# Kernel optimization log

Measured on AMD Instinct MI355X. Metric: run time of the kernel, lower is better.

## Reference

```python
import jax, jax.numpy as jnp
import numpy as np

NUM_HEADS = 8
HEAD_SPLITS = [2, 3, 3]            # heads per crpe window {3:2, 5:3, 7:3}
WINDOWS = [3, 5, 7]


def dwconv(x, w, b, pad):
    """Depthwise conv. x: [B,C,H,W], w: [C,1,kh,kw] (OIHW), b: [C]."""
    y = jax.lax.conv_general_dilated(
        x, w, window_strides=(1, 1), padding=[(pad, pad), (pad, pad)],
        dimension_numbers=("NCHW", "OIHW", "NCHW"),
        feature_group_count=x.shape[1])
    return y + b[None, :, None, None]


def layernorm(x, w, b, eps=1e-6):
    m = jnp.mean(x, axis=-1, keepdims=True)
    v = jnp.mean(jnp.square(x - m), axis=-1, keepdims=True)
    return (x - m) * jax.lax.rsqrt(v + eps) * w + b


def setup_inputs() -> dict:
    key = jax.random.key(0)
    ks = jax.random.split(key, 16)
    B, Hs, Ws, C = 16, 56, 56, 512
    N = Hs * Ws
    Ch = C // NUM_HEADS
    hid = int(C * 4.0)

    def rn(k, shape, s=0.02):
        return jax.random.normal(k, shape, jnp.float32) * s

    return {
        "x": jax.random.normal(ks[0], (B, N, C), jnp.float32),
        "H": Hs, "W": Ws,
        "cpe_w": rn(ks[1], (C, 1, 3, 3)), "cpe_b": jnp.zeros((C,), jnp.float32),
        "ln1_w": jnp.ones((C,), jnp.float32), "ln1_b": jnp.zeros((C,), jnp.float32),
        "qkv_w": rn(ks[2], (C, 3 * C)),
        "proj_w": rn(ks[3], (C, C)), "proj_b": jnp.zeros((C,), jnp.float32),
        "w3": rn(ks[4], (HEAD_SPLITS[0] * Ch, 1, 3, 3)), "b3": jnp.zeros((HEAD_SPLITS[0] * Ch,), jnp.float32),
        "w5": rn(ks[5], (HEAD_SPLITS[1] * Ch, 1, 5, 5)), "b5": jnp.zeros((HEAD_SPLITS[1] * Ch,), jnp.float32),
        "w7": rn(ks[6], (HEAD_SPLITS[2] * Ch, 1, 7, 7)), "b7": jnp.zeros((HEAD_SPLITS[2] * Ch,), jnp.float32),
        "ln2_w": jnp.ones((C,), jnp.float32), "ln2_b": jnp.zeros((C,), jnp.float32),
        "fc1_w": rn(ks[7], (C, hid)), "fc1_b": jnp.zeros((hid,), jnp.float32),
        "fc2_w": rn(ks[8], (hid, C)), "fc2_b": jnp.zeros((C,), jnp.float32),
    }


def reference(x, H, W, cpe_w, cpe_b, ln1_w, ln1_b, qkv_w, proj_w, proj_b,
              w3, b3, w5, b5, w7, b7, ln2_w, ln2_b, fc1_w, fc1_b, fc2_w, fc2_b):
    B, N, C = x.shape
    h = NUM_HEADS
    Ch = C // h
    scale = Ch ** -0.5

    # --- ConvPosEnc (no cls token: N == H*W branch) ---
    feat = jnp.transpose(x, (0, 2, 1)).reshape(B, C, H, W)
    feat = dwconv(feat, cpe_w, cpe_b, pad=1) + feat
    x0 = jnp.transpose(feat.reshape(B, C, N), (0, 2, 1))  # [B,N,C]

    # --- FactorAttnConvRelPosEnc ---
    cur = layernorm(x0, ln1_w, ln1_b)
    qkv = (cur @ qkv_w).reshape(B, N, 3, h, Ch)
    qkv = jnp.transpose(qkv, (2, 0, 3, 1, 4))  # [3,B,h,N,Ch]
    q, k, v = qkv[0], qkv[1], qkv[2]

    k_sm = jax.nn.softmax(k, axis=2)                    # softmax over tokens
    kv = jnp.einsum("bhnk,bhnv->bhkv", k_sm, v)         # [B,h,Ch,Ch]
    factor_att = jnp.einsum("bhnk,bhkv->bhnv", q, kv)   # [B,h,N,Ch]

    # ConvRelPosEnc: grouped depthwise convs on v per head split
    v_img = jnp.transpose(v, (0, 1, 3, 2)).reshape(B, h * Ch, H, W)
    c0, c1 = HEAD_SPLITS[0] * Ch, (HEAD_SPLITS[0] + HEAD_SPLITS[1]) * Ch
    conv_v = jnp.concatenate([
        dwconv(v_img[:, :c0], w3, b3, pad=1),
        dwconv(v_img[:, c0:c1], w5, b5, pad=2),
        dwconv(v_img[:, c1:], w7, b7, pad=3),
    ], axis=1)
    conv_v = jnp.transpose(conv_v.reshape(B, h, Ch, N), (0, 1, 3, 2))  # [B,h,N,Ch]
    crpe = q * conv_v

    attn = scale * factor_att + crpe
    attn = jnp.transpose(attn, (0, 2, 1, 3)).reshape(B, N, C)
    attn = attn @ proj_w + proj_b

    x0 = x0 + attn

    # --- FFN ---
    cur = layernorm(x0, ln2_w, ln2_b)
    hdn = jax.nn.gelu(cur @ fc1_w + fc1_b, approximate=False)
    out = x0 + (hdn @ fc2_w + fc2_b)
    return out
```

## Files before the change

kernel.cpp:

```cpp
#include <hip/hip_runtime.h>
#include <hip/hip_bf16.h>

typedef unsigned short ushort_t;
typedef unsigned int uint_t;

typedef float f32x4 __attribute__((ext_vector_type(4)));
typedef short s16x8 __attribute__((ext_vector_type(8)));

#define HW 56
#define NTOK 3136
#define CDIM 512
#define NHEAD 8
#define CH 64
#define QKVC 1536
#define HID 2048
#define NSEG 28
#define SEGLEN 112

#define WPK_TOTAL 19976

__device__ __forceinline__ float b2f(ushort_t u) {
    union { uint_t i; float f; } cv; cv.i = ((uint_t)u) << 16; return cv.f;
}
__device__ __forceinline__ ushort_t f2b(float f) {
    union { __hip_bfloat16 h; ushort_t u; } cv; cv.h = __float2bfloat16(f); return cv.u;
}
__device__ __forceinline__ uint_t pk2(float a, float b) {
    return (uint_t)f2b(a) | ((uint_t)f2b(b) << 16);
}

__device__ __forceinline__ float gelu_fast(float x) {
    float u = x * 0.7978845608f * (1.f + 0.044715f * x * x);
    u = fminf(fmaxf(u, -10.f), 10.f);
    float e = __expf(2.f * u);
    float th = (e - 1.f) / (e + 1.f);
    return 0.5f * x * (1.f + th);
}

__device__ __forceinline__ void gload_lds16(const ushort_t* g, ushort_t* l) {
    __builtin_amdgcn_global_load_lds(
        (const __attribute__((address_space(1))) void*)g,
        (__attribute__((address_space(3))) void*)l, 16, 0, 0);
}

__global__ __launch_bounds__(256) void k_transpose(const float* __restrict__ in,
                                                   ushort_t* __restrict__ out,
                                                   int K, int Npr) {
    __shared__ float tile[32][33];
    int tx = threadIdx.x & 31, ty = threadIdx.x >> 5;
    int kb = blockIdx.y * 32, nb = blockIdx.x * 32;
#pragma unroll
    for (int i = 0; i < 4; i++)
        tile[ty + i * 8][tx] = in[(size_t)(kb + ty + i * 8) * Npr + nb + tx];
    __syncthreads();
#pragma unroll
    for (int i = 0; i < 4; i++)
        out[(size_t)(nb + ty + i * 8) * K + kb + tx] = f2b(tile[tx][ty + i * 8]);
}

__global__ __launch_bounds__(256) void k_wtrans(const float* __restrict__ cpe_w,
                                                const float* __restrict__ w3,
                                                const float* __restrict__ w5,
                                                const float* __restrict__ w7,
                                                float* __restrict__ wpk) {
    int idx = blockIdx.x * 256 + threadIdx.x;
    if (idx < 4608) {
        int i = idx / 512, c = idx % 512;
        wpk[idx] = cpe_w[c * 9 + i];
    } else if (idx < 5760) {
        int r = idx - 4608; int i = r / 128, c = r % 128;
        wpk[idx] = w3[c * 9 + i];
    } else if (idx < 10560) {
        int r = idx - 5760; int i = r / 192, c = r % 192;
        wpk[idx] = w5[c * 25 + i];
    } else if (idx < 19968) {
        int r = idx - 10560; int i = r / 192, c = r % 192;
        wpk[idx] = w7[c * 49 + i];
    } else if (idx < WPK_TOTAL) {
        wpk[idx] = 0.f;
    }
}

__global__ __launch_bounds__(256) void k_cpe_ln(const float* __restrict__ x,
                                                const float* __restrict__ wpk,
                                                const float* __restrict__ bias,
                                                const float* __restrict__ lnw,
                                                const float* __restrict__ lnb,
                                                float* __restrict__ x0,
                                                ushort_t* __restrict__ cur) {
    int t = threadIdx.x;
    int tok = t >> 7;
    int tl = t & 127;
    int c0 = tl * 4;
    int bb = blockIdx.y;
    int n = blockIdx.x * 2 + tok;
    int y = n / HW, xx = n % HW;
    const float* xb = x + ((size_t)bb * NTOK) * CDIM + c0;
    const float* zf = wpk + 19968;
    float4 a = *(const float4*)(bias + c0);
#pragma unroll
    for (int i = 0; i < 9; i++) {
        int ky = i / 3 - 1, kx = i % 3 - 1;
        int yy = y + ky, xc = xx + kx;
        bool ok = (unsigned)yy < HW && (unsigned)xc < HW;
        const float* ap = ok ? (xb + (size_t)(yy * HW + xc) * CDIM) : zf;
        float4 d = *(const float4*)ap;
        float4 w = *(const float4*)(wpk + i * 512 + c0);
        a.x += w.x * d.x; a.y += w.y * d.y; a.z += w.z * d.z; a.w += w.w * d.w;
    }
    float4 ctr = *(const float4*)(xb + (size_t)n * CDIM);
    a.x += ctr.x; a.y += ctr.y; a.z += ctr.z; a.w += ctr.w;
    *(float4*)(x0 + ((size_t)bb * NTOK + n) * CDIM + c0) = a;

    float s = a.x + a.y + a.z + a.w;
    float s2 = a.x * a.x + a.y * a.y + a.z * a.z + a.w * a.w;
#pragma unroll
    for (int m = 1; m < 64; m <<= 1) { s += __shfl_xor(s, m); s2 += __shfl_xor(s2, m); }
    __shared__ float rs[4], rs2[4];
    int wid = t >> 6, lane = t & 63;
    if (lane == 0) { rs[wid] = s; rs2[wid] = s2; }
    __syncthreads();
    s = rs[tok * 2] + rs[tok * 2 + 1];
    s2 = rs2[tok * 2] + rs2[tok * 2 + 1];
    float mean = s * (1.f / CDIM);
    float var = s2 * (1.f / CDIM) - mean * mean;
    float rstd = rsqrtf(var + 1e-6f);
    float4 wv = *(const float4*)(lnw + c0);
    float4 bv = *(const float4*)(lnb + c0);
    float o0 = (a.x - mean) * rstd * wv.x + bv.x;
    float o1 = (a.y - mean) * rstd * wv.y + bv.y;
    float o2 = (a.z - mean) * rstd * wv.z + bv.z;
    float o3 = (a.w - mean) * rstd * wv.w + bv.w;
    uint2 ro; ro.x = pk2(o0, o1); ro.y = pk2(o2, o3);
    *(uint2*)(cur + ((size_t)bb * NTOK + n) * CDIM + c0) = ro;
}

__global__ __launch_bounds__(256) void k_ln(const float* __restrict__ in,
                                            const float* __restrict__ w,
                                            const float* __restrict__ b,
                                            ushort_t* __restrict__ out) {
    int wid = threadIdx.x >> 6, lane = threadIdx.x & 63;
    size_t row = (size_t)blockIdx.x * 4 + wid;
    const float* p = in + row * CDIM + lane * 8;
    float4 v0 = *(const float4*)p;
    float4 v1 = *(const float4*)(p + 4);
    float v[8] = { v0.x, v0.y, v0.z, v0.w, v1.x, v1.y, v1.z, v1.w };
    float s = 0.f, s2 = 0.f;
#pragma unroll
    for (int i = 0; i < 8; i++) { s += v[i]; s2 += v[i] * v[i]; }
#pragma unroll
    for (int m = 1; m < 64; m <<= 1) { s += __shfl_xor(s, m); s2 += __shfl_xor(s2, m); }
    float mean = s * (1.f / CDIM);
    float var = s2 * (1.f / CDIM) - mean * mean;
    float rstd = rsqrtf(var + 1e-6f);
    float4 w0 = *(const float4*)(w + lane * 8);
    float4 w1 = *(const float4*)(w + lane * 8 + 4);
    float4 b0 = *(const float4*)(b + lane * 8);
    float4 b1 = *(const float4*)(b + lane * 8 + 4);
    float wv[8] = { w0.x, w0.y, w0.z, w0.w, w1.x, w1.y, w1.z, w1.w };
    float bv[8] = { b0.x, b0.y, b0.z, b0.w, b1.x, b1.y, b1.z, b1.w };
    float o[8];
#pragma unroll
    for (int i = 0; i < 8; i++) o[i] = (v[i] - mean) * rstd * wv[i] + bv[i];
    uint4 ro;
    ro.x = pk2(o[0], o[1]); ro.y = pk2(o[2], o[3]); ro.z = pk2(o[4], o[5]); ro.w = pk2(o[6], o[7]);
    *(uint4*)(out + row * CDIM + lane * 8) = ro;
}

template <int EPI>
__global__ __launch_bounds__(256, 3) void k_gemm(const ushort_t* __restrict__ A,
                                                 const ushort_t* __restrict__ Bt,
                                                 const float* __restrict__ bias,
                                                 const float* __restrict__ res,
                                                 void* __restrict__ outv,
                                                 int M, int Npr, int K) {
    __shared__ ushort_t As[128 * 64];
    __shared__ ushort_t Bs[128 * 64];
    int t = threadIdx.x;

    int gx = gridDim.x;
    int bx = blockIdx.x, by = blockIdx.y;
    int nwg = gx * gridDim.y;
    if ((nwg & 7) == 0) {
        int fid = by * gx + bx;
        int cpx = nwg >> 3;
        int swz = (fid & 7) * cpx + (fid >> 3);
        bx = swz % gx; by = swz / gx;
    }
    int m0 = by * 128, n0 = bx * 128;

    int wid = t >> 6, lane = t & 63, q = lane >> 4, r16 = lane & 15;
    int wr = wid >> 1, wc = wid & 1;
    f32x4 acc[4][4] = {};

    int srow = lane >> 3;
    int scol = ((lane & 7) ^ srow) * 8;
    const ushort_t* pA[4];
    const ushort_t* pB[4];
    int lofs[4];
#pragma unroll
    for (int c = 0; c < 4; c++) {
        int rowc = wid * 32 + c * 8 + srow;
        int ra = m0 + rowc; if (ra > M - 1) ra = M - 1;
        pA[c] = A + (size_t)ra * K + scol;
        pB[c] = Bt + (size_t)(n0 + rowc) * K + scol;
        lofs[c] = (wid * 32 + c * 8) * 64;
    }

    for (int k0 = 0; k0 < K; k0 += 64) {
#pragma unroll
        for (int c = 0; c < 4; c++) gload_lds16(pA[c] + k0, &As[lofs[c]]);
#pragma unroll
        for (int c = 0; c < 4; c++) gload_lds16(pB[c] + k0, &Bs[lofs[c]]);
        __syncthreads();
#pragma unroll
        for (int kk = 0; kk < 64; kk += 32) {
            s16x8 a[4], b[4];
#pragma unroll
            for (int i = 0; i < 4; i++) {
                int R = wr * 64 + i * 16 + r16;
                a[i] = *(const s16x8*)&As[R * 64 + ((kk + q * 8) ^ ((R & 7) * 8))];
            }
#pragma unroll
            for (int j = 0; j < 4; j++) {
                int S = wc * 64 + j * 16 + r16;
                b[j] = *(const s16x8*)&Bs[S * 64 + ((kk + q * 8) ^ ((S & 7) * 8))];
            }
#pragma unroll
            for (int mi = 0; mi < 4; mi++)
#pragma unroll
                for (int ni = 0; ni < 4; ni++)
                    acc[mi][ni] = __builtin_amdgcn_mfma_f32_16x16x32_bf16(a[mi], b[ni], acc[mi][ni], 0, 0, 0);
        }
        __syncthreads();
    }

#pragma unroll
    for (int mi = 0; mi < 4; mi++) {
#pragma unroll
        for (int ni = 0; ni < 4; ni++) {
            int col = n0 + wc * 64 + ni * 16 + r16;
            float bv = 0.f;
            if (EPI != 0) bv = bias[col];
#pragma unroll
            for (int r = 0; r < 4; r++) {
                int row = m0 + wr * 64 + mi * 16 + q * 4 + r;
                if (row >= M) continue;
                float xv = acc[mi][ni][r];
                size_t idx = (size_t)row * Npr + col;
                if (EPI == 0) {
                    ((ushort_t*)outv)[idx] = f2b(xv);
                } else if (EPI == 1) {
                    ((float*)outv)[idx] = xv + bv + res[idx];
                } else {
                    ((ushort_t*)outv)[idx] = f2b(gelu_fast(xv + bv));
                }
            }
        }
    }
}

__global__ __launch_bounds__(256) void k_sm_part(const ushort_t* __restrict__ qkv,
                                                 float* __restrict__ mxp,
                                                 float* __restrict__ ssp) {
    int cblk = blockIdx.x, seg = blockIdx.y, b = blockIdx.z;
    int ch = threadIdx.x & 63, nt = threadIdx.x >> 6;
    int c0 = cblk * 64;
    const ushort_t* base = qkv + (size_t)b * NTOK * QKVC + CDIM + c0 + ch;
    int nbeg = seg * SEGLEN, nend = nbeg + SEGLEN;
    __shared__ float redm[4][64], reds[4][64];
    float mx = -1e30f, sum = 0.f;
    for (int n = nbeg + nt; n < nend; n += 4) {
        float v = b2f(base[(size_t)n * QKVC]);
        float mn = fmaxf(mx, v);
        sum = sum * __expf(mx - mn) + __expf(v - mn);
        mx = mn;
    }
    redm[nt][ch] = mx;
    reds[nt][ch] = sum;
    __syncthreads();
    if (nt == 0) {
        float m = fmaxf(fmaxf(redm[0][ch], redm[1][ch]), fmaxf(redm[2][ch], redm[3][ch]));
        float S = reds[0][ch] * __expf(redm[0][ch] - m)
                + reds[1][ch] * __expf(redm[1][ch] - m)
                + reds[2][ch] * __expf(redm[2][ch] - m)
                + reds[3][ch] * __expf(redm[3][ch] - m);
        size_t o = ((size_t)b * CDIM + c0 + ch) * NSEG + seg;
        mxp[o] = m;
        ssp[o] = S;
    }
}

__global__ __launch_bounds__(512) void k_sm_red(const float* __restrict__ mxp,
                                                const float* __restrict__ ssp,
                                                float* __restrict__ Mx,
                                                float* __restrict__ Sx) {
    int b = blockIdx.x, c = threadIdx.x;
    const float* mp = mxp + ((size_t)b * CDIM + c) * NSEG;
    const float* sp = ssp + ((size_t)b * CDIM + c) * NSEG;
    float m = -1e30f;
#pragma unroll 4
    for (int s = 0; s < NSEG; s++) m = fmaxf(m, mp[s]);
    float S = 0.f;
#pragma unroll 4
    for (int s = 0; s < NSEG; s++) S += sp[s] * __expf(mp[s] - m);
    Mx[b * CDIM + c] = m;
    Sx[b * CDIM + c] = S;
}

__global__ __launch_bounds__(256) void k_kv_part(const ushort_t* __restrict__ qkv,
                                                 const float* __restrict__ Mx,
                                                 float* __restrict__ kvpart) {
    int hd = blockIdx.x, seg = blockIdx.y, b = blockIdx.z;
    int c0 = hd * CH;
    int t = threadIdx.x, tx = t & 15, ty = t >> 4;
    __shared__ float mx[64];
    __shared__ float ek[8][64];
    __shared__ float vv[8][64];
    if (t < 64) mx[t] = Mx[b * CDIM + c0 + t];
    __syncthreads();
    float acc[4][4] = {};
    const ushort_t* kbase = qkv + (size_t)b * NTOK * QKVC + CDIM + c0;
    const ushort_t* vbase = kbase + CDIM;
    int nbeg = seg * SEGLEN;
    for (int n0 = nbeg; n0 < nbeg + SEGLEN; n0 += 8) {
        for (int idx = t; idx < 512; idx += 256) {
            int r = idx >> 6, ch = idx & 63;
            ek[r][ch] = __expf(b2f(kbase[(size_t)(n0 + r) * QKVC + ch]) - mx[ch]);
            vv[r][ch] = b2f(vbase[(size_t)(n0 + r) * QKVC + ch]);
        }
        __syncthreads();
#pragma unroll
        for (int r = 0; r < 8; r++) {
            float ekv[4], vvv[4];
#pragma unroll
            for (int i = 0; i < 4; i++) ekv[i] = ek[r][ty * 4 + i];
#pragma unroll
            for (int j = 0; j < 4; j++) vvv[j] = vv[r][tx * 4 + j];
#pragma unroll
            for (int i = 0; i < 4; i++)
#pragma unroll
                for (int j = 0; j < 4; j++) acc[i][j] += ekv[i] * vvv[j];
        }
        __syncthreads();
    }
    float* outp = kvpart + (((size_t)(b * NHEAD + hd)) * NSEG + seg) * 4096;
#pragma unroll
    for (int i = 0; i < 4; i++)
#pragma unroll
        for (int j = 0; j < 4; j++)
            outp[(size_t)(ty * 4 + i) * CH + tx * 4 + j] = acc[i][j];
}

__global__ __launch_bounds__(256) void k_kv_red(const float* __restrict__ kvpart,
                                                const float* __restrict__ Sx,
                                                float* __restrict__ kv) {
    int quad = blockIdx.x, hd = blockIdx.y, b = blockIdx.z;
    int bh = b * NHEAD + hd;
    int t = threadIdx.x;
    const float* basep = kvpart + ((size_t)bh * NSEG) * 4096 + quad * 1024;
    const float scale = 0.125f;
#pragma unroll
    for (int k = 0; k < 4; k++) {
        int e = k * 256 + t;
        float s = 0.f;
        for (int sg = 0; sg < NSEG; sg++) s += basep[(size_t)sg * 4096 + e];
        int ck = (quad * 1024 + e) >> 6;
        float sinv = scale / Sx[b * CDIM + hd * CH + ck];
        kv[(size_t)bh * 4096 + quad * 1024 + e] = s * sinv;
    }
}

template <int KS>
__global__ __launch_bounds__(KS == 3 ? 256 : 192) void k_conv(const ushort_t* __restrict__ qkv,
                                                              const float* __restrict__ wpk,
                                                              const float* __restrict__ bias,
                                                              ushort_t* __restrict__ conv) {
    constexpr int PAD = KS / 2;
    constexpr int CHBASE = (KS == 3) ? 0 : ((KS == 5) ? 128 : 320);
    constexpr int WBASE = (KS == 3) ? 4608 : ((KS == 5) ? 5760 : 10560);
    constexpr int WSTR = (KS == 3) ? 128 : 192;
    constexpr int GRP = (KS == 3) ? 16 : 24;
    constexpr int LANES = (KS == 3) ? 16 : 8;
    int t = threadIdx.x;
    int g = t % GRP;
    int tl = t / GRP;
    int bb = blockIdx.y;
    int n0 = blockIdx.x * (LANES * 4) + tl * 4;
    int crel = g * 8;
    const ushort_t* vb = qkv + (size_t)bb * NTOK * QKVC + 2 * CDIM + CHBASE + crel;
    const ushort_t* zp = (const ushort_t*)(wpk + 19968);
    float4 blo = *(const float4*)(bias + crel);
    float4 bhi = *(const float4*)(bias + crel + 4);
    float acc[4][8];
    int ty[4], txx[4];
#pragma unroll
    for (int k4 = 0; k4 < 4; k4++) {
        int n = n0 + k4; ty[k4] = n / HW; txx[k4] = n % HW;
        acc[k4][0] = blo.x; acc[k4][1] = blo.y; acc[k4][2] = blo.z; acc[k4][3] = blo.w;
        acc[k4][4] = bhi.x; acc[k4][5] = bhi.y; acc[k4][6] = bhi.z; acc[k4][7] = bhi.w;
    }
    int ky = -PAD, kx = -PAD;
#pragma unroll 1
    for (int i = 0; i < KS * KS; i++) {
        const float* wp = wpk + WBASE + i * WSTR + crel;
        float4 wlo = *(const float4*)wp;
        float4 whi = *(const float4*)(wp + 4);
        float w[8] = { wlo.x, wlo.y, wlo.z, wlo.w, whi.x, whi.y, whi.z, whi.w };
#pragma unroll
        for (int k4 = 0; k4 < 4; k4++) {
            int yy = ty[k4] + ky, xc = txx[k4] + kx;
            bool ok = (unsigned)yy < HW && (unsigned)xc < HW;
            const ushort_t* ap = ok ? (vb + (size_t)(yy * HW + xc) * QKVC) : zp;
            uint4 d = *(const uint4*)ap;
            float dv[8];
            dv[0] = b2f((ushort_t)(d.x & 0xffff)); dv[1] = b2f((ushort_t)(d.x >> 16));
            dv[2] = b2f((ushort_t)(d.y & 0xffff)); dv[3] = b2f((ushort_t)(d.y >> 16));
            dv[4] = b2f((ushort_t)(d.z & 0xffff)); dv[5] = b2f((ushort_t)(d.z >> 16));
            dv[6] = b2f((ushort_t)(d.w & 0xffff)); dv[7] = b2f((ushort_t)(d.w >> 16));
#pragma unroll
            for (int j = 0; j < 8; j++) acc[k4][j] += w[j] * dv[j];
        }
        kx++; if (kx > PAD) { kx = -PAD; ky++; }
    }
#pragma unroll
    for (int k4 = 0; k4 < 4; k4++) {
        int n = n0 + k4;
        uint4 o;
        o.x = pk2(acc[k4][0], acc[k4][1]);
        o.y = pk2(acc[k4][2], acc[k4][3]);
        o.z = pk2(acc[k4][4], acc[k4][5]);
        o.w = pk2(acc[k4][6], acc[k4][7]);
        *(uint4*)&conv[((size_t)bb * NTOK + n) * CDIM + CHBASE + crel] = o;
    }
}

__global__ __launch_bounds__(256) void k_attn(const ushort_t* __restrict__ qkv,
                                              const float* __restrict__ kv,
                                              ushort_t* __restrict__ conv) {
    int nb = blockIdx.x, hd = blockIdx.y, b = blockIdx.z;
    int t = threadIdx.x, tx = t & 15, ty = t >> 4;
    __shared__ float kvl[64 * 64];
    __shared__ float ql[64 * 65];
    const float* kvsrc = kv + (size_t)(b * NHEAD + hd) * CH * CH;
    for (int idx = t; idx < 4096; idx += 256) kvl[idx] = kvsrc[idx];
    const ushort_t* qbase = qkv + ((size_t)b * NTOK + nb * 64) * QKVC + hd * CH;
    for (int idx = t; idx < 4096; idx += 256) {
        int r = idx >> 6, ck = idx & 63;
        ql[r * 65 + ck] = b2f(qbase[(size_t)r * QKVC + ck]);
    }
    __syncthreads();
    float acc[4][4] = {};
    for (int ck = 0; ck < 64; ck++) {
        float kvr[4];
#pragma unroll
        for (int j = 0; j < 4; j++) kvr[j] = kvl[ck * 64 + tx * 4 + j];
#pragma unroll
        for (int i = 0; i < 4; i++) {
            float qv = ql[(ty + 16 * i) * 65 + ck];
#pragma unroll
            for (int j = 0; j < 4; j++) acc[i][j] += qv * kvr[j];
        }
    }
    size_t obase = (size_t)b * NTOK + nb * 64;
#pragma unroll
    for (int i = 0; i < 4; i++) {
        int row = ty + 16 * i;
        size_t o = (obase + row) * CDIM + hd * CH + tx * 4;
        uint2 cv = *(const uint2*)&conv[o];
        float c0 = b2f((ushort_t)(cv.x & 0xffff)), c1 = b2f((ushort_t)(cv.x >> 16));
        float c2 = b2f((ushort_t)(cv.y & 0xffff)), c3 = b2f((ushort_t)(cv.y >> 16));
        float q0 = ql[row * 65 + tx * 4 + 0];
        float q1 = ql[row * 65 + tx * 4 + 1];
        float q2 = ql[row * 65 + tx * 4 + 2];
        float q3 = ql[row * 65 + tx * 4 + 3];
        uint2 ov;
        ov.x = pk2(acc[i][0] + q0 * c0, acc[i][1] + q1 * c1);
        ov.y = pk2(acc[i][2] + q2 * c2, acc[i][3] + q3 * c3);
        *(uint2*)&conv[o] = ov;
    }
}

extern "C" void kernel_launch(void* const* d_in, const int* in_sizes, int n_in,
                              void* d_out, int out_size, void* d_ws, size_t ws_size,
                              hipStream_t stream) {
    const float* x     = (const float*)d_in[0];
    const float* cpe_w = (const float*)d_in[3];
    const float* cpe_b = (const float*)d_in[4];
    const float* ln1_w = (const float*)d_in[5];
    const float* ln1_b = (const float*)d_in[6];
    const float* qkv_w = (const float*)d_in[7];
    const float* proj_w = (const float*)d_in[8];
    const float* proj_b = (const float*)d_in[9];
    const float* w3 = (const float*)d_in[10];
    const float* b3 = (const float*)d_in[11];
    const float* w5 = (const float*)d_in[12];
    const float* b5 = (const float*)d_in[13];
    const float* w7 = (const float*)d_in[14];
    const float* b7 = (const float*)d_in[15];
    const float* ln2_w = (const float*)d_in[16];
    const float* ln2_b = (const float*)d_in[17];
    const float* fc1_w = (const float*)d_in[18];
    const float* fc1_b = (const float*)d_in[19];
    const float* fc2_w = (const float*)d_in[20];
    const float* fc2_b = (const float*)d_in[21];
    float* out = (float*)d_out;

    char* p = (char*)d_ws;
    ushort_t* wt_qkv  = (ushort_t*)p; p += (size_t)QKVC * CDIM * 2;
    ushort_t* wt_proj = (ushort_t*)p; p += (size_t)CDIM * CDIM * 2;
    ushort_t* wt_fc1  = (ushort_t*)p; p += (size_t)HID * CDIM * 2;
    ushort_t* wt_fc2  = (ushort_t*)p; p += (size_t)CDIM * HID * 2;
    float* wpk = (float*)p; p += 20480 * 4;
    size_t wt_bytes = (size_t)(p - (char*)d_ws);

    k_transpose<<<dim3(QKVC / 32, CDIM / 32), 256, 0, stream>>>(qkv_w, wt_qkv, CDIM, QKVC);
    k_transpose<<<dim3(CDIM / 32, CDIM / 32), 256, 0, stream>>>(proj_w, wt_proj, CDIM, CDIM);
    k_transpose<<<dim3(HID / 32, CDIM / 32), 256, 0, stream>>>(fc1_w, wt_fc1, CDIM, HID);
    k_transpose<<<dim3(CDIM / 32, HID / 32), 256, 0, stream>>>(fc2_w, wt_fc2, HID, CDIM);
    k_wtrans<<<(WPK_TOTAL + 255) / 256, 256, 0, stream>>>(cpe_w, w3, w5, w7, wpk);

    const size_t per_b = (size_t)NTOK * CDIM * 2
                       + (size_t)NTOK * HID * 2
                       + (size_t)NHEAD * CH * CH * 4
                       + (size_t)NHEAD * NSEG * 4096 * 4
                       + (size_t)CDIM * 4 * 2
                       + (size_t)CDIM * NSEG * 4 * 2;
    int Bc = 16;
    while (Bc > 1 && wt_bytes + (size_t)Bc * per_b > ws_size) Bc >>= 1;

    ushort_t* cur = (ushort_t*)p; p += (size_t)Bc * NTOK * CDIM * 2;
    char* un = p;                 p += (size_t)Bc * NTOK * HID * 2;
    ushort_t* conv = (ushort_t*)un;
    ushort_t* qkvb = (ushort_t*)(un + (size_t)Bc * NTOK * CDIM * 2);
    ushort_t* hid  = (ushort_t*)un;
    float* kvb    = (float*)p; p += (size_t)Bc * NHEAD * CH * CH * 4;
    float* kvpart = (float*)p; p += (size_t)Bc * NHEAD * NSEG * 4096 * 4;
    float* Mx  = (float*)p; p += (size_t)Bc * CDIM * 4;
    float* Sx  = (float*)p; p += (size_t)Bc * CDIM * 4;
    float* mxp = (float*)p; p += (size_t)Bc * CDIM * NSEG * 4;
    float* ssp = (float*)p;

    for (int b0 = 0; b0 < 16; b0 += Bc) {
        int M = Bc * NTOK;
        int gy = (M + 127) / 128;
        const float* xch = x + (size_t)b0 * NTOK * CDIM;
        float* och = out + (size_t)b0 * NTOK * CDIM;
        float* x0 = och;

        k_cpe_ln<<<dim3(NTOK / 2, Bc), 256, 0, stream>>>(xch, wpk, cpe_b, ln1_w, ln1_b, x0, cur);
        k_gemm<0><<<dim3(QKVC / 128, gy), 256, 0, stream>>>(cur, wt_qkv, nullptr, nullptr, qkvb, M, QKVC, CDIM);
        k_sm_part<<<dim3(8, NSEG, Bc), 256, 0, stream>>>(qkvb, mxp, ssp);
        k_sm_red<<<Bc, 512, 0, stream>>>(mxp, ssp, Mx, Sx);
        k_kv_part<<<dim3(NHEAD, NSEG, Bc), 256, 0, stream>>>(qkvb, Mx, kvpart);
        k_kv_red<<<dim3(4, NHEAD, Bc), 256, 0, stream>>>(kvpart, Sx, kvb);
        k_conv<3><<<dim3(NTOK / 64, Bc), 256, 0, stream>>>(qkvb, wpk, b3, conv);
        k_conv<5><<<dim3(NTOK / 32, Bc), 192, 0, stream>>>(qkvb, wpk, b5, conv);
        k_conv<7><<<dim3(NTOK / 32, Bc), 192, 0, stream>>>(qkvb, wpk, b7, conv);
        k_attn<<<dim3(NTOK / 64, NHEAD, Bc), 256, 0, stream>>>(qkvb, kvb, conv);
        k_gemm<1><<<dim3(CDIM / 128, gy), 256, 0, stream>>>(conv, wt_proj, proj_b, x0, x0, M, CDIM, CDIM);
        k_ln<<<M / 4, 256, 0, stream>>>(x0, ln2_w, ln2_b, cur);
        k_gemm<2><<<dim3(HID / 128, gy), 256, 0, stream>>>(cur, wt_fc1, fc1_b, nullptr, hid, M, HID, CDIM);
        k_gemm<1><<<dim3(CDIM / 128, gy), 256, 0, stream>>>(hid, wt_fc2, fc2_b, x0, och, M, CDIM, HID);
    }
}
```

Before: 1.235 ms.

## Fuse softmax stats into kv partial kernel with per-segment max rescaling

Computes the per-segment key max and sum inside k_kv_part and uses the local segment max for exponentiation, instead of running separate softmax-partial and softmax-reduce kernels first. The kv reduction kernel then rescales each segment's partial kv by exp(local max minus global max) and divides by the combined sum. This removes two kernel launches and one extra read pass over the key columns. In exchange, k_kv_red does a little more work per element and k_kv_part gains an extra synchronisation.

```diff
diff --git a/kernel.cpp b/kernel.cpp
--- a/kernel.cpp
+++ b/kernel.cpp
@@ -260,74 +260,53 @@
     }
 }
 
-__global__ __launch_bounds__(256) void k_sm_part(const ushort_t* __restrict__ qkv,
+__global__ __launch_bounds__(256) void k_kv_part(const ushort_t* __restrict__ qkv,
                                                  float* __restrict__ mxp,
-                                                 float* __restrict__ ssp) {
-    int cblk = blockIdx.x, seg = blockIdx.y, b = blockIdx.z;
-    int ch = threadIdx.x & 63, nt = threadIdx.x >> 6;
-    int c0 = cblk * 64;
-    const ushort_t* base = qkv + (size_t)b * NTOK * QKVC + CDIM + c0 + ch;
-    int nbeg = seg * SEGLEN, nend = nbeg + SEGLEN;
-    __shared__ float redm[4][64], reds[4][64];
-    float mx = -1e30f, sum = 0.f;
-    for (int n = nbeg + nt; n < nend; n += 4) {
-        float v = b2f(base[(size_t)n * QKVC]);
-        float mn = fmaxf(mx, v);
-        sum = sum * __expf(mx - mn) + __expf(v - mn);
-        mx = mn;
-    }
-    redm[nt][ch] = mx;
-    reds[nt][ch] = sum;
-    __syncthreads();
-    if (nt == 0) {
-        float m = fmaxf(fmaxf(redm[0][ch], redm[1][ch]), fmaxf(redm[2][ch], redm[3][ch]));
-        float S = reds[0][ch] * __expf(redm[0][ch] - m)
-                + reds[1][ch] * __expf(redm[1][ch] - m)
-                + reds[2][ch] * __expf(redm[2][ch] - m)
-                + reds[3][ch] * __expf(redm[3][ch] - m);
-        size_t o = ((size_t)b * CDIM + c0 + ch) * NSEG + seg;
-        mxp[o] = m;
-        ssp[o] = S;
-    }
-}
-
-__global__ __launch_bounds__(512) void k_sm_red(const float* __restrict__ mxp,
-                                                const float* __restrict__ ssp,
-                                                float* __restrict__ Mx,
-                                                float* __restrict__ Sx) {
-    int b = blockIdx.x, c = threadIdx.x;
-    const float* mp = mxp + ((size_t)b * CDIM + c) * NSEG;
-    const float* sp = ssp + ((size_t)b * CDIM + c) * NSEG;
-    float m = -1e30f;
-#pragma unroll 4
-    for (int s = 0; s < NSEG; s++) m = fmaxf(m, mp[s]);
-    float S = 0.f;
-#pragma unroll 4
-    for (int s = 0; s < NSEG; s++) S += sp[s] * __expf(mp[s] - m);
-    Mx[b * CDIM + c] = m;
-    Sx[b * CDIM + c] = S;
-}
-
-__global__ __launch_bounds__(256) void k_kv_part(const ushort_t* __restrict__ qkv,
-                                                 const float* __restrict__ Mx,
+                                                 float* __restrict__ ssp,
                                                  float* __restrict__ kvpart) {
     int hd = blockIdx.x, seg = blockIdx.y, b = blockIdx.z;
     int c0 = hd * CH;
     int t = threadIdx.x, tx = t & 15, ty = t >> 4;
+    int ch = t & 63, nt4 = t >> 6;
     __shared__ float mx[64];
     __shared__ float ek[8][64];
     __shared__ float vv[8][64];
-    if (t < 64) mx[t] = Mx[b * CDIM + c0 + t];
-    __syncthreads();
-    float acc[4][4] = {};
+    __shared__ float redm[4][64], reds[4][64];
     const ushort_t* kbase = qkv + (size_t)b * NTOK * QKVC + CDIM + c0;
     const ushort_t* vbase = kbase + CDIM;
     int nbeg = seg * SEGLEN;
+
+    {
+        const ushort_t* kb = kbase + ch;
+        float m = -1e30f, s = 0.f;
+        for (int n = nbeg + nt4; n < nbeg + SEGLEN; n += 4) {
+            float v = b2f(kb[(size_t)n * QKVC]);
+            float mn = fmaxf(m, v);
+            s = s * __expf(m - mn) + __expf(v - mn);
+            m = mn;
+        }
+        redm[nt4][ch] = m; reds[nt4][ch] = s;
+    }
+    __syncthreads();
+    if (t < 64) {
+        float m = fmaxf(fmaxf(redm[0][t], redm[1][t]), fmaxf(redm[2][t], redm[3][t]));
+        float S = reds[0][t] * __expf(redm[0][t] - m)
+                + reds[1][t] * __expf(redm[1][t] - m)
+                + reds[2][t] * __expf(redm[2][t] - m)
+                + reds[3][t] * __expf(redm[3][t] - m);
+        mx[t] = m;
+        size_t o = ((size_t)b * CDIM + c0 + t) * NSEG + seg;
+        mxp[o] = m;
+        ssp[o] = S;
+    }
+    __syncthreads();
+
+    float acc[4][4] = {};
     for (int n0 = nbeg; n0 < nbeg + SEGLEN; n0 += 8) {
         for (int idx = t; idx < 512; idx += 256) {
-            int r = idx >> 6, ch = idx & 63;
-            ek[r][ch] = __expf(b2f(kbase[(size_t)(n0 + r) * QKVC + ch]) - mx[ch]);
-            vv[r][ch] = b2f(vbase[(size_t)(n0 + r) * QKVC + ch]);
+            int r = idx >> 6, chh = idx & 63;
+            ek[r][chh] = __expf(b2f(kbase[(size_t)(n0 + r) * QKVC + chh]) - mx[chh]);
+            vv[r][chh] = b2f(vbase[(size_t)(n0 + r) * QKVC + chh]);
         }
         __syncthreads();
 #pragma unroll
@@ -353,21 +332,38 @@
 }
 
 __global__ __launch_bounds__(256) void k_kv_red(const float* __restrict__ kvpart,
-                                                const float* __restrict__ Sx,
+                                                const float* __restrict__ mxp,
+                                                const float* __restrict__ ssp,
                                                 float* __restrict__ kv) {
     int quad = blockIdx.x, hd = blockIdx.y, b = blockIdx.z;
     int bh = b * NHEAD + hd;
     int t = threadIdx.x;
+    __shared__ float ef[NSEG][64];
+    __shared__ float sinv[64];
+    if (t < 64) {
+        const float* mp = mxp + ((size_t)b * CDIM + hd * CH + t) * NSEG;
+        const float* sp = ssp + ((size_t)b * CDIM + hd * CH + t) * NSEG;
+        float m = -1e30f;
+#pragma unroll 4
+        for (int s = 0; s < NSEG; s++) m = fmaxf(m, mp[s]);
+        float S = 0.f;
+#pragma unroll 4
+        for (int s = 0; s < NSEG; s++) {
+            float e = __expf(mp[s] - m);
+            ef[s][t] = e;
+            S += sp[s] * e;
+        }
+        sinv[t] = 0.125f / S;
+    }
+    __syncthreads();
     const float* basep = kvpart + ((size_t)bh * NSEG) * 4096 + quad * 1024;
-    const float scale = 0.125f;
 #pragma unroll
     for (int k = 0; k < 4; k++) {
         int e = k * 256 + t;
+        int ck = (quad * 1024 + e) >> 6;
         float s = 0.f;
-        for (int sg = 0; sg < NSEG; sg++) s += basep[(size_t)sg * 4096 + e];
-        int ck = (quad * 1024 + e) >> 6;
-        float sinv = scale / Sx[b * CDIM + hd * CH + ck];
-        kv[(size_t)bh * 4096 + quad * 1024 + e] = s * sinv;
+        for (int sg = 0; sg < NSEG; sg++) s += basep[(size_t)sg * 4096 + e] * ef[sg][ck];
+        kv[(size_t)bh * 4096 + quad * 1024 + e] = s * sinv[ck];
     }
 }
 
@@ -524,7 +520,6 @@
                        + (size_t)NTOK * HID * 2
                        + (size_t)NHEAD * CH * CH * 4
                        + (size_t)NHEAD * NSEG * 4096 * 4
-                       + (size_t)CDIM * 4 * 2
                        + (size_t)CDIM * NSEG * 4 * 2;
     int Bc = 16;
     while (Bc > 1 && wt_bytes + (size_t)Bc * per_b > ws_size) Bc >>= 1;
@@ -536,8 +531,6 @@
     ushort_t* hid  = (ushort_t*)un;
     float* kvb    = (float*)p; p += (size_t)Bc * NHEAD * CH * CH * 4;
     float* kvpart = (float*)p; p += (size_t)Bc * NHEAD * NSEG * 4096 * 4;
-    float* Mx  = (float*)p; p += (size_t)Bc * CDIM * 4;
-    float* Sx  = (float*)p; p += (size_t)Bc * CDIM * 4;
     float* mxp = (float*)p; p += (size_t)Bc * CDIM * NSEG * 4;
     float* ssp = (float*)p;
 
@@ -550,10 +543,8 @@
 
         k_cpe_ln<<<dim3(NTOK / 2, Bc), 256, 0, stream>>>(xch, wpk, cpe_b, ln1_w, ln1_b, x0, cur);
         k_gemm<0><<<dim3(QKVC / 128, gy), 256, 0, stream>>>(cur, wt_qkv, nullptr, nullptr, qkvb, M, QKVC, CDIM);
-        k_sm_part<<<dim3(8, NSEG, Bc), 256, 0, stream>>>(qkvb, mxp, ssp);
-        k_sm_red<<<Bc, 512, 0, stream>>>(mxp, ssp, Mx, Sx);
-        k_kv_part<<<dim3(NHEAD, NSEG, Bc), 256, 0, stream>>>(qkvb, Mx, kvpart);
-        k_kv_red<<<dim3(4, NHEAD, Bc), 256, 0, stream>>>(kvpart, Sx, kvb);
+        k_kv_part<<<dim3(NHEAD, NSEG, Bc), 256, 0, stream>>>(qkvb, mxp, ssp, kvpart);
+        k_kv_red<<<dim3(4, NHEAD, Bc), 256, 0, stream>>>(kvpart, mxp, ssp, kvb);
         k_conv<3><<<dim3(NTOK / 64, Bc), 256, 0, stream>>>(qkvb, wpk, b3, conv);
         k_conv<5><<<dim3(NTOK / 32, Bc), 192, 0, stream>>>(qkvb, wpk, b5, conv);
         k_conv<7><<<dim3(NTOK / 32, Bc), 192, 0, stream>>>(qkvb, wpk, b7, conv);
```

Result: no change. 1.210 ms (-2.0%).
